# Kernel optimization log

Measured on AMD Instinct MI355X. Metric: run time of the kernel, lower is better.

Reference implementation:

```python
import jax, jax.numpy as jnp
import numpy as np

N_AGENTS = 10000
N_TARGETS = 10000
N_EDGES = 320000
IN_CH = 8
DS = 32          # n_channels // 2 per GAT preprocessor
NCH = 64         # n_channels
C = 128          # 2 * n_channels hidden width
OUT = 2
N_TAPS = 3
N_LAYERS = 2
RADIUS = 2.0
K_NBR = 10       # max_num_neighbors in radius_graph
BIG = 1e9


def radius_nbrs(qpos, kpos, radius, k, exclude_self):
    """For each query point, indices of <=k nearest key points within radius."""
    d2 = jnp.sum((qpos[:, None, :] - kpos[None, :, :]) ** 2, axis=-1)  # [Nq, Nk]
    if exclude_self:
        n = qpos.shape[0]
        d2 = d2.at[jnp.arange(n), jnp.arange(n)].set(BIG)
    d2 = jnp.where(d2 <= radius * radius, d2, BIG)
    negv, idx = jax.lax.top_k(-d2, k)   # nearest-k (deterministic stand-in for PyG's first-k)
    valid = negv > -BIG * 0.5           # [Nq, k] True where a real in-radius neighbor
    return idx, valid


def gatv2(src_feats, dst_feats, idx, valid, Wl, Wr, att, b):
    """Single-head GATv2Conv over a fixed-K neighbor list (idx indexes src_feats)."""
    xl = src_feats @ Wl                      # [Ns, H] messages
    xr = dst_feats @ Wr                      # [Nd, H]
    g = jax.nn.leaky_relu(xl[idx] + xr[:, None, :], 0.2)   # [Nd, K, H]
    s = jnp.einsum('nkh,h->nk', g, att)
    s = jnp.where(valid, s, -BIG)
    s = s - jnp.max(s, axis=1, keepdims=True)
    p = jnp.exp(s) * valid                   # masked exp; isolated nodes -> all-zero
    alpha = p / (jnp.sum(p, axis=1, keepdims=True) + 1e-16)
    return jnp.einsum('nk,nkh->nh', alpha, xl[idx]) + b


def graph_filter(x, src, dst, W, b, n):
    """Polynomial graph filter: y = sum_k S^k x W_k + b, S = unweighted adjacency."""
    y = x @ W[0]
    h = x
    for k in range(1, W.shape[0]):
        h = jax.ops.segment_sum(h[src], dst, num_segments=n)  # one shift tap
        y = y + h @ W[k]
    return y + b


def setup_inputs() -> dict:
    key = jax.random.key(0)
    ks = jax.random.split(key, 16)
    f32 = jnp.float32
    return {
        'own_obs': jax.random.normal(ks[0], (N_AGENTS, IN_CH), dtype=f32),
        'agent_positions': jax.random.uniform(ks[1], (N_AGENTS, 2), dtype=f32) * 100.0,
        'target_positions': jax.random.uniform(ks[2], (N_TARGETS, 2), dtype=f32) * 100.0,
        'W_self': jax.random.normal(ks[3], (IN_CH, NCH), dtype=f32) * 0.1,
        'b_self': jnp.zeros((NCH,), f32),
        'ag_Wl': jax.random.normal(ks[4], (2, DS), dtype=f32) * 0.1,
        'ag_Wr': jax.random.normal(ks[5], (2, DS), dtype=f32) * 0.1,
        'ag_att': jax.random.normal(ks[6], (DS,), dtype=f32) * 0.1,
        'ag_b': jnp.zeros((DS,), f32),
        'tg_Wl': jax.random.normal(ks[7], (2, DS), dtype=f32) * 0.1,
        'tg_Wr': jax.random.normal(ks[8], (2, DS), dtype=f32) * 0.1,
        'tg_att': jax.random.normal(ks[9], (DS,), dtype=f32) * 0.1,
        'tg_b': jnp.zeros((DS,), f32),
        'gf_W': jax.random.normal(ks[10], (N_LAYERS, N_TAPS + 1, C, C), dtype=f32) * (1.0 / np.sqrt(C)),
        'gf_b': jnp.zeros((N_LAYERS, C), f32),
        'bn_gamma': jnp.ones((N_LAYERS, C), f32),
        'bn_beta': jnp.zeros((N_LAYERS, C), f32),
        'W_read': jax.random.normal(ks[11], (C, OUT), dtype=f32) * 0.1,
        'b_read': jnp.zeros((OUT,), f32),
        'edge_index': jax.random.randint(ks[12], (2, N_EDGES), 0, N_AGENTS, dtype=jnp.int32),
    }


def reference(own_obs, agent_positions, target_positions, W_self, b_self,
              ag_Wl, ag_Wr, ag_att, ag_b, tg_Wl, tg_Wr, tg_att, tg_b,
              gf_W, gf_b, bn_gamma, bn_beta, W_read, b_read, edge_index):
    n = agent_positions.shape[0]
    # dynamic radius graphs (agent-agent; target->agent)
    a_idx, a_valid = radius_nbrs(agent_positions, agent_positions, RADIUS, K_NBR, True)
    t_idx, t_valid = radius_nbrs(agent_positions, target_positions, RADIUS, K_NBR, False)

    s = own_obs @ W_self + b_self                                            # self MLP (1 layer)
    a = gatv2(agent_positions, agent_positions, a_idx, a_valid, ag_Wl, ag_Wr, ag_att, ag_b)
    t = gatv2(target_positions, agent_positions, t_idx, t_valid, tg_Wl, tg_Wr, tg_att, tg_b)
    x = jnp.concatenate([s, a, t], axis=1)                                   # [N, 128]

    src, dst = edge_index[0], edge_index[1]
    for l in range(N_LAYERS):
        h = graph_filter(x, src, dst, gf_W[l], gf_b[l], n)
        mu = jnp.mean(h, axis=0)
        var = jnp.var(h, axis=0)
        h = (h - mu) / jnp.sqrt(var + 1e-5) * bn_gamma[l] + bn_beta[l]       # BatchNorm
        x = x + jax.nn.leaky_relu(h, 0.01)                                   # residual block
    return x @ W_read + b_read
```

## Files before the change

### kernel.cpp

```cpp
#include <hip/hip_runtime.h>

typedef unsigned long long u64;
typedef unsigned int u32;
typedef unsigned short ushort_t;

#define NA 10000
#define NE 320000
#define KN 10
#define GRID 50
#define NCELL (GRID * GRID)

typedef __attribute__((ext_vector_type(8))) short short8v;
typedef __attribute__((ext_vector_type(4))) float f32x4;

__device__ __forceinline__ u32 f2bf(float f) {
  union { float f; u32 u; } v; v.f = f;
  return (v.u + 0x7fffu + ((v.u >> 16) & 1u)) >> 16;
}
__device__ __forceinline__ float bf2f(u32 b) {
  union { u32 u; float f; } v; v.u = b << 16;
  return v.f;
}

__device__ __forceinline__ void insert10(u64* top, u64 key) {
#pragma unroll
  for (int t = 9; t > 0; --t) {
    u64 prev = top[t - 1];
    u64 cur = top[t];
    top[t] = (key < prev) ? prev : ((key < cur) ? key : cur);
  }
  top[0] = (key < top[0]) ? key : top[0];
}

__device__ __forceinline__ int cell_of(float2 p) {
  int cx = (int)(p.x * 0.5f);
  int cy = (int)(p.y * 0.5f);
  cx = min(max(cx, 0), GRID - 1);
  cy = min(max(cy, 0), GRID - 1);
  return cy * GRID + cx;
}

__global__ __launch_bounds__(256) void k_hist_self(const int* __restrict__ edst,
                                                   const float2* __restrict__ apos,
                                                   const float2* __restrict__ tpos,
                                                   int* __restrict__ deg, int* __restrict__ chist,
                                                   const float* __restrict__ own_obs,
                                                   const float* __restrict__ W_self, const float* __restrict__ b_self,
                                                   float* __restrict__ x,
                                                   const float* __restrict__ gfW,
                                                   ushort_t* __restrict__ Wh, ushort_t* __restrict__ Wlo) {
  __shared__ float sW[512], sb[64];
  int t = threadIdx.x;
  for (int i = t; i < 512; i += 256) sW[i] = W_self[i];
  if (t < 64) sb[t] = b_self[t];
  __syncthreads();
  int i = blockIdx.x * 256 + t;
  if (i < NE) {
    atomicAdd(&deg[edst[i]], 1);
  } else if (i < NE + 2 * NA) {
    int ii = i - NE;
    int graph = (ii >= NA) ? 1 : 0;
    int idx = ii - graph * NA;
    float2 p = graph ? tpos[idx] : apos[idx];
    atomicAdd(&chist[graph * NCELL + cell_of(p)], 1);
  } else if (i < NE + 2 * NA + 8 * NA) {
    int gid = i - NE - 2 * NA;
    int q = gid >> 3;
    int c8 = (gid & 7) * 8;
    const float4* op = (const float4*)(own_obs + (size_t)q * 8);
    float4 o0 = op[0], o1 = op[1];
    float obs[8] = {o0.x, o0.y, o0.z, o0.w, o1.x, o1.y, o1.z, o1.w};
    float out[8];
#pragma unroll
    for (int jj = 0; jj < 8; ++jj) {
      int c = c8 + jj;
      float s = sb[c];
#pragma unroll
      for (int k = 0; k < 8; ++k) s += obs[k] * sW[k * 64 + c];
      out[jj] = s;
    }
    float* xrow = x + (size_t)q * 128 + c8;
    *(float4*)(xrow) = make_float4(out[0], out[1], out[2], out[3]);
    *(float4*)(xrow + 4) = make_float4(out[4], out[5], out[6], out[7]);
  } else if (i < NE + 2 * NA + 8 * NA + 131072) {
    int w = i - NE - 2 * NA - 8 * NA;
    int l = w >> 16;
    int rem = w & 65535;
    int tt = rem >> 14;
    int k = (rem >> 7) & 127;
    int n = rem & 127;
    float v = gfW[(size_t)w];
    int kt = k >> 5;
    int hi = (k >> 3) & 3;
    int j = k & 7;
    int ct = n >> 4;
    int lane = hi * 16 + (n & 15);
    size_t dst = (((((size_t)(l * 4 + tt) * 4 + kt) * 8 + ct) * 64 + lane) * 8 + j);
    u32 h = f2bf(v);
    float r = v - bf2f(h);
    Wh[dst] = (ushort_t)h;
    Wlo[dst] = (ushort_t)f2bf(r);
  }
}

__global__ __launch_bounds__(1024) void k_scan_all(const int* __restrict__ deg, int* __restrict__ rp,
                                                   const int* __restrict__ chist, int* __restrict__ crp) {
  __shared__ int part[1024];
  int t = threadIdx.x;
  const int* in;
  int* out;
  int per, tot;
  if (blockIdx.x == 0) { in = deg; out = rp; per = 10; tot = NA; }
  else { in = chist; out = crp; per = 5; tot = 2 * NCELL; }
  int beg = min(t * per, tot), end = min(beg + per, tot);
  int s = 0;
  for (int i = beg; i < end; ++i) s += in[i];
  part[t] = s;
  __syncthreads();
  for (int o = 1; o < 1024; o <<= 1) {
    int v = part[t];
    int u = (t >= o) ? part[t - o] : 0;
    __syncthreads();
    part[t] = v + u;
    __syncthreads();
  }
  int base = (t > 0) ? part[t - 1] : 0;
  for (int i = beg; i < end; ++i) { out[i] = base; base += in[i]; }
  if (t == 1023) out[tot] = part[1023];
}

__global__ __launch_bounds__(256) void k_scatter_all(const int* __restrict__ esrc, const int* __restrict__ edst,
                                                     const int* __restrict__ rp, int* __restrict__ cur,
                                                     int* __restrict__ col,
                                                     const float2* __restrict__ apos, const float2* __restrict__ tpos,
                                                     const int* __restrict__ crp, int* __restrict__ ccur,
                                                     float2* __restrict__ ps, int* __restrict__ pid) {
  int i = blockIdx.x * 256 + threadIdx.x;
  if (i < NE) {
    int d = edst[i];
    int p = atomicAdd(&cur[d], 1);
    col[rp[d] + p] = esrc[i];
  } else if (i < NE + 2 * NA) {
    int ii = i - NE;
    int graph = (ii >= NA) ? 1 : 0;
    int idx = ii - graph * NA;
    float2 p = graph ? tpos[idx] : apos[idx];
    int gc = graph * NCELL + cell_of(p);
    int o = crp[gc] + atomicAdd(&ccur[gc], 1);
    ps[o] = p;
    pid[o] = idx;
  }
}

__global__ __launch_bounds__(256) void k_nbr_gat(const float2* __restrict__ apos, const float2* __restrict__ tpos,
                                                 const int* __restrict__ crp,
                                                 const float2* __restrict__ ps, const int* __restrict__ pid,
                                                 const float* __restrict__ agWl, const float* __restrict__ agWr,
                                                 const float* __restrict__ agatt, const float* __restrict__ agb,
                                                 const float* __restrict__ tgWl, const float* __restrict__ tgWr,
                                                 const float* __restrict__ tgatt, const float* __restrict__ tgb,
                                                 float* __restrict__ x) {
  __shared__ float sWl[2][64], sWr[2][64], satt[2][32], sbb[2][32];
  int t = threadIdx.x;
  if (t < 64) { sWl[0][t] = agWl[t]; sWr[0][t] = agWr[t]; sWl[1][t] = tgWl[t]; sWr[1][t] = tgWr[t]; }
  else if (t < 96) {
    int u = t - 64;
    satt[0][u] = agatt[u]; sbb[0][u] = agb[u]; satt[1][u] = tgatt[u]; sbb[1][u] = tgb[u];
  }
  __syncthreads();
  int tid = blockIdx.x * 256 + t;
  if (tid >= 2 * NA) return;
  int graph = (tid >= NA) ? 1 : 0;
  int q = tid - graph * NA;
  float2 qp = apos[q];
  int cx = min(max((int)(qp.x * 0.5f), 0), GRID - 1);
  int cy = min(max((int)(qp.y * 0.5f), 0), GRID - 1);

  u64 top[10];
#pragma unroll
  for (int k = 0; k < 10; ++k) top[k] = ~0ull;

  int x0 = max(cx - 1, 0), x1 = min(cx + 1, GRID - 1);
  int y0 = max(cy - 1, 0), y1 = min(cy + 1, GRID - 1);
  for (int yy = y0; yy <= y1; ++yy) {
    int cb = graph * NCELL + yy * GRID + x0;
    int ce = graph * NCELL + yy * GRID + x1;
    int b = crp[cb], e = crp[ce + 1];
    for (int j = b; j < e; ++j) {
      float2 kp = ps[j];
      float dx = qp.x - kp.x;
      float dy = qp.y - kp.y;
      float d2 = __fadd_rn(__fmul_rn(dx, dx), __fmul_rn(dy, dy));
      int g = pid[j];
      if (d2 <= 4.0f && !(graph == 0 && g == q)) {
        u64 key = ((u64)__float_as_uint(d2) << 32) | (u32)g;
        if (key < top[9]) insert10(top, key);
      }
    }
  }
  int cnt = 0;
#pragma unroll
  for (int k = 0; k < 10; ++k) cnt += (top[k] != ~0ull) ? 1 : 0;
  int idx[10];
#pragma unroll
  for (int k = 0; k < 10; ++k) idx[k] = (k < cnt) ? (int)(u32)(top[k] & 0xffffffffu) : 0;

  const float2* srcpos = graph ? tpos : apos;
  const float* wl = sWl[graph];
  const float* wr = sWr[graph];
  const float* at = satt[graph];
  const float* bb = sbb[graph];
  float xr[32];
#pragma unroll
  for (int c = 0; c < 32; ++c) xr[c] = qp.x * wr[c] + qp.y * wr[32 + c];
  float pv[10];
  float m = -1e30f;
#pragma unroll
  for (int k = 0; k < 10; ++k) {
    float2 p = srcpos[idx[k]];
    float s = 0.f;
#pragma unroll
    for (int c = 0; c < 32; ++c) {
      float xl = p.x * wl[c] + p.y * wl[32 + c];
      float g = xl + xr[c];
      g = (g >= 0.f) ? g : 0.2f * g;
      s += at[c] * g;
    }
    pv[k] = s;
    m = (k < cnt) ? fmaxf(m, s) : m;
  }
  float sum = 0.f;
#pragma unroll
  for (int k = 0; k < 10; ++k) {
    float e = (k < cnt) ? expf(pv[k] - m) : 0.f;
    pv[k] = e;
    sum += e;
  }
  float inv = 1.f / (sum + 1e-16f);
  float out[32];
#pragma unroll
  for (int c = 0; c < 32; ++c) out[c] = bb[c];
#pragma unroll
  for (int k = 0; k < 10; ++k) {
    float a = pv[k] * inv;
    float2 p = srcpos[idx[k]];
#pragma unroll
    for (int c = 0; c < 32; ++c) {
      float xl = p.x * wl[c] + p.y * wl[32 + c];
      out[c] += a * xl;
    }
  }
  float* xrow = x + (size_t)q * 128 + (graph ? 96 : 64);
#pragma unroll
  for (int c4 = 0; c4 < 8; ++c4)
    *(float4*)(xrow + c4 * 4) = make_float4(out[c4 * 4], out[c4 * 4 + 1], out[c4 * 4 + 2], out[c4 * 4 + 3]);
}

__global__ __launch_bounds__(256) void k_shift4(const float* __restrict__ xin, float* __restrict__ xout,
                                                const int* __restrict__ rp, const int* __restrict__ col) {
  int bid = blockIdx.x;
  int half = (bid & 7) >> 2;
  int slot = (bid >> 3) * 4 + (bid & 3);
  if (slot >= 1250) return;
  int hw = threadIdx.x >> 5;
  int li = threadIdx.x & 31;
  int row = slot * 8 + hw;
  int beg = rp[row], end = rp[row + 1];
  const float2* x2 = (const float2*)xin;
  int base = half * 32 + li;
  float2 acc = {0.f, 0.f};
  int j = beg;
  for (; j + 3 < end; j += 4) {
    int s0 = col[j], s1 = col[j + 1], s2 = col[j + 2], s3 = col[j + 3];
    float2 v0 = x2[(size_t)s0 * 64 + base];
    float2 v1 = x2[(size_t)s1 * 64 + base];
    float2 v2 = x2[(size_t)s2 * 64 + base];
    float2 v3 = x2[(size_t)s3 * 64 + base];
    acc.x += v0.x; acc.y += v0.y;
    acc.x += v1.x; acc.y += v1.y;
    acc.x += v2.x; acc.y += v2.y;
    acc.x += v3.x; acc.y += v3.y;
  }
  for (; j < end; ++j) {
    float2 v = x2[(size_t)col[j] * 64 + base];
    acc.x += v.x; acc.y += v.y;
  }
  ((float2*)xout)[(size_t)row * 64 + base] = acc;
}

__global__ __launch_bounds__(256) void k_gemm_mfma3(const float* __restrict__ a0, const float* __restrict__ a1,
                                                    const float* __restrict__ a2, const float* __restrict__ a3,
                                                    const ushort_t* __restrict__ Wh, const ushort_t* __restrict__ Wlo,
                                                    const float* __restrict__ b, float* __restrict__ y,
                                                    double* __restrict__ parts) {
  const int lane = threadIdx.x & 63;
  const int wave = threadIdx.x >> 6;
  const int ct0 = wave * 2;
  const int row = lane & 15;
  const int hi = lane >> 4;
  const int rb = blockIdx.x * 16;

  f32x4 acc[2];
#pragma unroll
  for (int c = 0; c < 2; ++c) {
    float bv = b[(ct0 + c) * 16 + row];
    acc[c][0] = bv; acc[c][1] = bv; acc[c][2] = bv; acc[c][3] = bv;
  }

  const float* aps[4] = {a0, a1, a2, a3};
#pragma unroll
  for (int t = 0; t < 4; ++t) {
    const float* at = aps[t];
#pragma unroll
    for (int kt = 0; kt < 4; ++kt) {
      const float* ap = at + (size_t)(rb + row) * 128 + kt * 32 + hi * 8;
      float4 fa = *(const float4*)(ap);
      float4 fb = *(const float4*)(ap + 4);
      float av[8] = {fa.x, fa.y, fa.z, fa.w, fb.x, fb.y, fb.z, fb.w};
      short8v ah, al;
#pragma unroll
      for (int j = 0; j < 8; ++j) {
        u32 h = f2bf(av[j]);
        float r = av[j] - bf2f(h);
        ah[j] = (short)h;
        al[j] = (short)f2bf(r);
      }
#pragma unroll
      for (int c = 0; c < 2; ++c) {
        size_t widx = ((((size_t)t * 4 + kt) * 8 + (ct0 + c)) * 64 + lane) * 8;
        short8v bh = *(const short8v*)(Wh + widx);
        short8v bl = *(const short8v*)(Wlo + widx);
        acc[c] = __builtin_amdgcn_mfma_f32_16x16x32_bf16(ah, bh, acc[c], 0, 0, 0);
        acc[c] = __builtin_amdgcn_mfma_f32_16x16x32_bf16(al, bh, acc[c], 0, 0, 0);
        acc[c] = __builtin_amdgcn_mfma_f32_16x16x32_bf16(ah, bl, acc[c], 0, 0, 0);
      }
    }
  }

#pragma unroll
  for (int c = 0; c < 2; ++c) {
#pragma unroll
    for (int r = 0; r < 4; ++r) {
      int grow = rb + hi * 4 + r;
      y[(size_t)grow * 128 + (ct0 + c) * 16 + row] = acc[c][r];
    }
  }

#pragma unroll
  for (int c = 0; c < 2; ++c) {
    double s = 0.0, ss = 0.0;
#pragma unroll
    for (int r = 0; r < 4; ++r) {
      double v = (double)acc[c][r];
      s += v;
      ss += v * v;
    }
    s += __shfl_xor(s, 16);
    ss += __shfl_xor(ss, 16);
    s += __shfl_xor(s, 32);
    ss += __shfl_xor(ss, 32);
    if (hi == 0) {
      int ch = (ct0 + c) * 16 + row;
      parts[(size_t)ch * 625 + blockIdx.x] = s;
      parts[(size_t)(128 + ch) * 625 + blockIdx.x] = ss;
    }
  }
}

__global__ __launch_bounds__(256) void k_bnfin(const double* __restrict__ parts,
                                               const float* __restrict__ gamma, const float* __restrict__ beta,
                                               float* __restrict__ AB) {
  __shared__ double s0[256], s1[256];
  int ch = blockIdx.x;
  int t = threadIdx.x;
  const double* ps = parts + (size_t)ch * 625;
  const double* pq = parts + (size_t)(128 + ch) * 625;
  double a = 0.0, b = 0.0;
  for (int i = t; i < 625; i += 256) { a += ps[i]; b += pq[i]; }
  s0[t] = a;
  s1[t] = b;
  __syncthreads();
  for (int o = 128; o > 0; o >>= 1) {
    if (t < o) { s0[t] += s0[t + o]; s1[t] += s1[t + o]; }
    __syncthreads();
  }
  if (t == 0) {
    double mu = s0[0] / (double)NA;
    double var = s1[0] / (double)NA - mu * mu;
    double rs = 1.0 / sqrt(var + 1e-5);
    AB[ch] = (float)rs * gamma[ch];
    AB[128 + ch] = beta[ch] - (float)(mu * rs) * gamma[ch];
  }
}

__global__ __launch_bounds__(256) void k_bnapply(const float* __restrict__ y, const float* __restrict__ AB,
                                                 const float* __restrict__ Wread, const float* __restrict__ bread,
                                                 float* __restrict__ x, float* __restrict__ out, int doread) {
  __shared__ float sAB[256], sWr[256];
  int t = threadIdx.x;
  sAB[t] = AB[t];
  sWr[t] = Wread[t];
  __syncthreads();
  const int n4 = NA * 32;
  for (int i = blockIdx.x * 256 + t; i < n4; i += gridDim.x * 256) {
    float4 yv = ((const float4*)y)[i];
    int c = (i & 31) * 4;
    float v0 = yv.x * sAB[c + 0] + sAB[128 + c + 0];
    float v1 = yv.y * sAB[c + 1] + sAB[128 + c + 1];
    float v2 = yv.z * sAB[c + 2] + sAB[128 + c + 2];
    float v3 = yv.w * sAB[c + 3] + sAB[128 + c + 3];
    v0 = (v0 >= 0.f) ? v0 : 0.01f * v0;
    v1 = (v1 >= 0.f) ? v1 : 0.01f * v1;
    v2 = (v2 >= 0.f) ? v2 : 0.01f * v2;
    v3 = (v3 >= 0.f) ? v3 : 0.01f * v3;
    float4 xv = ((float4*)x)[i];
    xv.x += v0; xv.y += v1; xv.z += v2; xv.w += v3;
    ((float4*)x)[i] = xv;
    if (doread) {
      float a0 = xv.x * sWr[(c + 0) * 2] + xv.y * sWr[(c + 1) * 2] + xv.z * sWr[(c + 2) * 2] + xv.w * sWr[(c + 3) * 2];
      float a1 = xv.x * sWr[(c + 0) * 2 + 1] + xv.y * sWr[(c + 1) * 2 + 1] + xv.z * sWr[(c + 2) * 2 + 1] + xv.w * sWr[(c + 3) * 2 + 1];
#pragma unroll
      for (int o = 1; o < 32; o <<= 1) {
        a0 += __shfl_xor(a0, o);
        a1 += __shfl_xor(a1, o);
      }
      if ((i & 31) == 0) {
        int row = i >> 5;
        out[row * 2 + 0] = a0 + bread[0];
        out[row * 2 + 1] = a1 + bread[1];
      }
    }
  }
}

extern "C" void kernel_launch(void* const* d_in, const int* in_sizes, int n_in,
                              void* d_out, int out_size, void* d_ws, size_t ws_size,
                              hipStream_t stream) {
  (void)in_sizes; (void)n_in; (void)out_size; (void)ws_size;
  const float* own_obs = (const float*)d_in[0];
  const float2* apos = (const float2*)d_in[1];
  const float2* tpos = (const float2*)d_in[2];
  const float* W_self = (const float*)d_in[3];
  const float* b_self = (const float*)d_in[4];
  const float* agWl = (const float*)d_in[5];
  const float* agWr = (const float*)d_in[6];
  const float* agatt = (const float*)d_in[7];
  const float* agb = (const float*)d_in[8];
  const float* tgWl = (const float*)d_in[9];
  const float* tgWr = (const float*)d_in[10];
  const float* tgatt = (const float*)d_in[11];
  const float* tgb = (const float*)d_in[12];
  const float* gfW = (const float*)d_in[13];
  const float* gfb = (const float*)d_in[14];
  const float* bng = (const float*)d_in[15];
  const float* bnb = (const float*)d_in[16];
  const float* Wread = (const float*)d_in[17];
  const float* bread = (const float*)d_in[18];
  const int* ei = (const int*)d_in[19];
  const int* esrc = ei;
  const int* edst = ei + NE;

  char* w = (char*)d_ws;
  size_t off = 0;
  auto take = [&](size_t bytes) -> void* {
    void* p = w + off;
    off += (bytes + 255) & ~(size_t)255;
    return p;
  };
  float* x = (float*)take((size_t)NA * 128 * 4);
  float* y = (float*)take((size_t)NA * 128 * 4);
  float* sh1 = (float*)take((size_t)NA * 128 * 4);
  float* sh2 = (float*)take((size_t)NA * 128 * 4);
  float* sh3 = (float*)take((size_t)NA * 128 * 4);
  ushort_t* Wh = (ushort_t*)take((size_t)131072 * 2);
  ushort_t* Wlo = (ushort_t*)take((size_t)131072 * 2);
  double* parts = (double*)take((size_t)256 * 625 * 8);
  float* AB = (float*)take(256 * 4);
  int* deg = (int*)take((size_t)NA * 4);
  int* cur = (int*)take((size_t)NA * 4);
  int* chist = (int*)take((size_t)2 * NCELL * 4);
  int* ccur = (int*)take((size_t)2 * NCELL * 4);
  int* rp = (int*)take((size_t)(NA + 1) * 4);
  int* col = (int*)take((size_t)NE * 4);
  int* crp = (int*)take((size_t)(2 * NCELL + 1) * 4);
  float2* ps = (float2*)take((size_t)2 * NA * 8);
  int* pid = (int*)take((size_t)2 * NA * 4);

  hipMemsetAsync(deg, 0, (size_t)((char*)(ccur + 2 * NCELL) - (char*)deg), stream);
  k_hist_self<<<(NE + 2 * NA + 8 * NA + 131072 + 255) / 256, 256, 0, stream>>>(
      edst, apos, tpos, deg, chist, own_obs, W_self, b_self, x, gfW, Wh, Wlo);
  k_scan_all<<<2, 1024, 0, stream>>>(deg, rp, chist, crp);
  k_scatter_all<<<(NE + 2 * NA + 255) / 256, 256, 0, stream>>>(esrc, edst, rp, cur, col,
                                                               apos, tpos, crp, ccur, ps, pid);
  k_nbr_gat<<<(2 * NA + 255) / 256, 256, 0, stream>>>(apos, tpos, crp, ps, pid,
                                                      agWl, agWr, agatt, agb, tgWl, tgWr, tgatt, tgb, x);

  for (int l = 0; l < 2; ++l) {
    const ushort_t* Whl = Wh + (size_t)l * 65536;
    const ushort_t* Wll = Wlo + (size_t)l * 65536;
    const float* bl = gfb + (size_t)l * 128;
    const float* gl = bng + (size_t)l * 128;
    const float* bb = bnb + (size_t)l * 128;
    k_shift4<<<2504, 256, 0, stream>>>(x, sh1, rp, col);
    k_shift4<<<2504, 256, 0, stream>>>(sh1, sh2, rp, col);
    k_shift4<<<2504, 256, 0, stream>>>(sh2, sh3, rp, col);
    k_gemm_mfma3<<<NA / 16, 256, 0, stream>>>(x, sh1, sh2, sh3, Whl, Wll, bl, y, parts);
    k_bnfin<<<128, 256, 0, stream>>>(parts, gl, bb, AB);
    k_bnapply<<<256, 256, 0, stream>>>(y, AB, Wread, bread, x, (float*)d_out, l == 1 ? 1 : 0);
  }
}
```

Before: 280.5 us.

## Widen shift gather to float4 per lane and process two row tiles per GEMM block

The sparse shift kernel now gathers 16-byte float4 chunks per lane, with 16 lanes covering half a row and four rows per wave, instead of float2 with 32 lanes per row. It also uses a 2-way unroll and a nontemporal store. The MFMA GEMM now computes 32 rows per block (two 16-row tiles), so each bf16 hi/lo weight fragment load is reused across two tiles. The partial-stat buffer shrinks to 313 blocks. This cuts weight reloads and instruction count per gathered byte, at the cost of more registers and fewer blocks for the GEMM.

```diff
diff --git a/kernel.cpp b/kernel.cpp
--- a/kernel.cpp
+++ b/kernel.cpp
@@ -9,6 +9,7 @@
 #define KN 10
 #define GRID 50
 #define NCELL (GRID * GRID)
+#define GB 313
 
 typedef __attribute__((ext_vector_type(8))) short short8v;
 typedef __attribute__((ext_vector_type(4))) float f32x4;
@@ -256,36 +257,31 @@
     *(float4*)(xrow + c4 * 4) = make_float4(out[c4 * 4], out[c4 * 4 + 1], out[c4 * 4 + 2], out[c4 * 4 + 3]);
 }
 
-__global__ __launch_bounds__(256) void k_shift4(const float* __restrict__ xin, float* __restrict__ xout,
+__global__ __launch_bounds__(256) void k_shift3(const float* __restrict__ xin, float* __restrict__ xout,
                                                 const int* __restrict__ rp, const int* __restrict__ col) {
   int bid = blockIdx.x;
   int half = (bid & 7) >> 2;
   int slot = (bid >> 3) * 4 + (bid & 3);
-  if (slot >= 1250) return;
-  int hw = threadIdx.x >> 5;
-  int li = threadIdx.x & 31;
-  int row = slot * 8 + hw;
+  if (slot >= 625) return;
+  int wid = threadIdx.x >> 6;
+  int lane = threadIdx.x & 63;
+  int q = lane >> 4;
+  int li = lane & 15;
+  int row = slot * 16 + wid * 4 + q;
   int beg = rp[row], end = rp[row + 1];
-  const float2* x2 = (const float2*)xin;
-  int base = half * 32 + li;
-  float2 acc = {0.f, 0.f};
+  const f32x4* x4 = (const f32x4*)xin;
+  int base = half * 16 + li;
+  f32x4 acc = {0.f, 0.f, 0.f, 0.f};
   int j = beg;
-  for (; j + 3 < end; j += 4) {
-    int s0 = col[j], s1 = col[j + 1], s2 = col[j + 2], s3 = col[j + 3];
-    float2 v0 = x2[(size_t)s0 * 64 + base];
-    float2 v1 = x2[(size_t)s1 * 64 + base];
-    float2 v2 = x2[(size_t)s2 * 64 + base];
-    float2 v3 = x2[(size_t)s3 * 64 + base];
-    acc.x += v0.x; acc.y += v0.y;
-    acc.x += v1.x; acc.y += v1.y;
-    acc.x += v2.x; acc.y += v2.y;
-    acc.x += v3.x; acc.y += v3.y;
-  }
-  for (; j < end; ++j) {
-    float2 v = x2[(size_t)col[j] * 64 + base];
-    acc.x += v.x; acc.y += v.y;
-  }
-  ((float2*)xout)[(size_t)row * 64 + base] = acc;
+  for (; j + 1 < end; j += 2) {
+    int s0 = col[j], s1 = col[j + 1];
+    f32x4 v0 = x4[(size_t)s0 * 32 + base];
+    f32x4 v1 = x4[(size_t)s1 * 32 + base];
+    acc += v0;
+    acc += v1;
+  }
+  if (j < end) acc += x4[(size_t)col[j] * 32 + base];
+  __builtin_nontemporal_store(acc, &((f32x4*)xout)[(size_t)row * 32 + base]);
 }
 
 __global__ __launch_bounds__(256) void k_gemm_mfma3(const float* __restrict__ a0, const float* __restrict__ a1,
@@ -298,13 +294,15 @@
   const int ct0 = wave * 2;
   const int row = lane & 15;
   const int hi = lane >> 4;
-  const int rb = blockIdx.x * 16;
-
-  f32x4 acc[2];
+  const int rb = blockIdx.x * 32;
+  const bool rt1ok = (rb + 16) < NA;
+
+  f32x4 acc[2][2];
 #pragma unroll
   for (int c = 0; c < 2; ++c) {
     float bv = b[(ct0 + c) * 16 + row];
-    acc[c][0] = bv; acc[c][1] = bv; acc[c][2] = bv; acc[c][3] = bv;
+    acc[0][c][0] = bv; acc[0][c][1] = bv; acc[0][c][2] = bv; acc[0][c][3] = bv;
+    acc[1][c][0] = bv; acc[1][c][1] = bv; acc[1][c][2] = bv; acc[1][c][3] = bv;
   }
 
   const float* aps[4] = {a0, a1, a2, a3};
@@ -313,36 +311,61 @@
     const float* at = aps[t];
 #pragma unroll
     for (int kt = 0; kt < 4; ++kt) {
-      const float* ap = at + (size_t)(rb + row) * 128 + kt * 32 + hi * 8;
-      float4 fa = *(const float4*)(ap);
-      float4 fb = *(const float4*)(ap + 4);
-      float av[8] = {fa.x, fa.y, fa.z, fa.w, fb.x, fb.y, fb.z, fb.w};
-      short8v ah, al;
-#pragma unroll
-      for (int j = 0; j < 8; ++j) {
-        u32 h = f2bf(av[j]);
-        float r = av[j] - bf2f(h);
-        ah[j] = (short)h;
-        al[j] = (short)f2bf(r);
+      short8v ah0, al0, ah1, al1;
+      {
+        const float* ap = at + (size_t)(rb + row) * 128 + kt * 32 + hi * 8;
+        float4 fa = *(const float4*)(ap);
+        float4 fb = *(const float4*)(ap + 4);
+        float av[8] = {fa.x, fa.y, fa.z, fa.w, fb.x, fb.y, fb.z, fb.w};
+#pragma unroll
+        for (int j = 0; j < 8; ++j) {
+          u32 h = f2bf(av[j]);
+          float r = av[j] - bf2f(h);
+          ah0[j] = (short)h;
+          al0[j] = (short)f2bf(r);
+        }
+      }
+      if (rt1ok) {
+        const float* ap = at + (size_t)(rb + 16 + row) * 128 + kt * 32 + hi * 8;
+        float4 fa = *(const float4*)(ap);
+        float4 fb = *(const float4*)(ap + 4);
+        float av[8] = {fa.x, fa.y, fa.z, fa.w, fb.x, fb.y, fb.z, fb.w};
+#pragma unroll
+        for (int j = 0; j < 8; ++j) {
+          u32 h = f2bf(av[j]);
+          float r = av[j] - bf2f(h);
+          ah1[j] = (short)h;
+          al1[j] = (short)f2bf(r);
+        }
+      } else {
+#pragma unroll
+        for (int j = 0; j < 8; ++j) { ah1[j] = 0; al1[j] = 0; }
       }
 #pragma unroll
       for (int c = 0; c < 2; ++c) {
         size_t widx = ((((size_t)t * 4 + kt) * 8 + (ct0 + c)) * 64 + lane) * 8;
         short8v bh = *(const short8v*)(Wh + widx);
         short8v bl = *(const short8v*)(Wlo + widx);
-        acc[c] = __builtin_amdgcn_mfma_f32_16x16x32_bf16(ah, bh, acc[c], 0, 0, 0);
-        acc[c] = __builtin_amdgcn_mfma_f32_16x16x32_bf16(al, bh, acc[c], 0, 0, 0);
-        acc[c] = __builtin_amdgcn_mfma_f32_16x16x32_bf16(ah, bl, acc[c], 0, 0, 0);
-      }
-    }
-  }
-
-#pragma unroll
-  for (int c = 0; c < 2; ++c) {
-#pragma unroll
-    for (int r = 0; r < 4; ++r) {
-      int grow = rb + hi * 4 + r;
-      y[(size_t)grow * 128 + (ct0 + c) * 16 + row] = acc[c][r];
+        acc[0][c] = __builtin_amdgcn_mfma_f32_16x16x32_bf16(ah0, bh, acc[0][c], 0, 0, 0);
+        acc[0][c] = __builtin_amdgcn_mfma_f32_16x16x32_bf16(al0, bh, acc[0][c], 0, 0, 0);
+        acc[0][c] = __builtin_amdgcn_mfma_f32_16x16x32_bf16(ah0, bl, acc[0][c], 0, 0, 0);
+        acc[1][c] = __builtin_amdgcn_mfma_f32_16x16x32_bf16(ah1, bh, acc[1][c], 0, 0, 0);
+        acc[1][c] = __builtin_amdgcn_mfma_f32_16x16x32_bf16(al1, bh, acc[1][c], 0, 0, 0);
+        acc[1][c] = __builtin_amdgcn_mfma_f32_16x16x32_bf16(ah1, bl, acc[1][c], 0, 0, 0);
+      }
+    }
+  }
+
+#pragma unroll
+  for (int rt = 0; rt < 2; ++rt) {
+    if (rt == 1 && !rt1ok) break;
+#pragma unroll
+    for (int c = 0; c < 2; ++c) {
+#pragma unroll
+      for (int r = 0; r < 4; ++r) {
+        int grow = rb + rt * 16 + hi * 4 + r;
+        y[(size_t)grow * 128 + (ct0 + c) * 16 + row] = acc[rt][c][r];
+      }
     }
   }
 
@@ -351,9 +374,17 @@
     double s = 0.0, ss = 0.0;
 #pragma unroll
     for (int r = 0; r < 4; ++r) {
-      double v = (double)acc[c][r];
+      double v = (double)acc[0][c][r];
       s += v;
       ss += v * v;
+    }
+    if (rt1ok) {
+#pragma unroll
+      for (int r = 0; r < 4; ++r) {
+        double v = (double)acc[1][c][r];
+        s += v;
+        ss += v * v;
+      }
     }
     s += __shfl_xor(s, 16);
     ss += __shfl_xor(ss, 16);
@@ -361,8 +392,8 @@
     ss += __shfl_xor(ss, 32);
     if (hi == 0) {
       int ch = (ct0 + c) * 16 + row;
-      parts[(size_t)ch * 625 + blockIdx.x] = s;
-      parts[(size_t)(128 + ch) * 625 + blockIdx.x] = ss;
+      parts[(size_t)ch * GB + blockIdx.x] = s;
+      parts[(size_t)(128 + ch) * GB + blockIdx.x] = ss;
     }
   }
 }
@@ -373,10 +404,10 @@
   __shared__ double s0[256], s1[256];
   int ch = blockIdx.x;
   int t = threadIdx.x;
-  const double* ps = parts + (size_t)ch * 625;
-  const double* pq = parts + (size_t)(128 + ch) * 625;
+  const double* ps = parts + (size_t)ch * GB;
+  const double* pq = parts + (size_t)(128 + ch) * GB;
   double a = 0.0, b = 0.0;
-  for (int i = t; i < 625; i += 256) { a += ps[i]; b += pq[i]; }
+  for (int i = t; i < GB; i += 256) { a += ps[i]; b += pq[i]; }
   s0[t] = a;
   s1[t] = b;
   __syncthreads();
@@ -474,7 +505,7 @@
   float* sh3 = (float*)take((size_t)NA * 128 * 4);
   ushort_t* Wh = (ushort_t*)take((size_t)131072 * 2);
   ushort_t* Wlo = (ushort_t*)take((size_t)131072 * 2);
-  double* parts = (double*)take((size_t)256 * 625 * 8);
+  double* parts = (double*)take((size_t)256 * GB * 8);
   float* AB = (float*)take(256 * 4);
   int* deg = (int*)take((size_t)NA * 4);
   int* cur = (int*)take((size_t)NA * 4);
@@ -501,10 +532,10 @@
     const float* bl = gfb + (size_t)l * 128;
     const float* gl = bng + (size_t)l * 128;
     const float* bb = bnb + (size_t)l * 128;
-    k_shift4<<<2504, 256, 0, stream>>>(x, sh1, rp, col);
-    k_shift4<<<2504, 256, 0, stream>>>(sh1, sh2, rp, col);
-    k_shift4<<<2504, 256, 0, stream>>>(sh2, sh3, rp, col);
-    k_gemm_mfma3<<<NA / 16, 256, 0, stream>>>(x, sh1, sh2, sh3, Whl, Wll, bl, y, parts);
+    k_shift3<<<1256, 256, 0, stream>>>(x, sh1, rp, col);
+    k_shift3<<<1256, 256, 0, stream>>>(sh1, sh2, rp, col);
+    k_shift3<<<1256, 256, 0, stream>>>(sh2, sh3, rp, col);
+    k_gemm_mfma3<<<GB, 256, 0, stream>>>(x, sh1, sh2, sh3, Whl, Wll, bl, y, parts);
     k_bnfin<<<128, 256, 0, stream>>>(parts, gl, bb, AB);
     k_bnapply<<<256, 256, 0, stream>>>(y, AB, Wread, bread, x, (float*)d_out, l == 1 ? 1 : 0);
   }
```

After: 259.6 us. -7.5%, faster.

## Fuse three shift taps into one cooperative kernel with grid syncs and float4 gathers

Applied to the files above, without the earlier changes.

Replaces the three separate shift-tap launches per layer with a single cooperative kernel that runs all three taps, separated by grid-wide syncs. The gather is widened from float2 to float4 per lane, with 16 lanes per row, and outputs are written with nontemporal stores. The aim is to remove two kernel launches and their gaps per layer and to issue fewer, wider memory requests. In exchange it depends on all 1256 blocks being co-resident, adds grid-sync cost, and unrolls the inner loop less deeply.

```diff
diff --git a/kernel.cpp b/kernel.cpp
--- a/kernel.cpp
+++ b/kernel.cpp
@@ -1,4 +1,7 @@
 #include <hip/hip_runtime.h>
+#include <hip/hip_cooperative_groups.h>
+
+namespace cg = cooperative_groups;
 
 typedef unsigned long long u64;
 typedef unsigned int u32;
@@ -9,6 +12,7 @@
 #define KN 10
 #define GRID 50
 #define NCELL (GRID * GRID)
+#define GB 625
 
 typedef __attribute__((ext_vector_type(8))) short short8v;
 typedef __attribute__((ext_vector_type(4))) float f32x4;
@@ -256,36 +260,42 @@
     *(float4*)(xrow + c4 * 4) = make_float4(out[c4 * 4], out[c4 * 4 + 1], out[c4 * 4 + 2], out[c4 * 4 + 3]);
 }
 
-__global__ __launch_bounds__(256) void k_shift4(const float* __restrict__ xin, float* __restrict__ xout,
-                                                const int* __restrict__ rp, const int* __restrict__ col) {
+__device__ __forceinline__ void shift_body(const float* __restrict__ xin, float* __restrict__ xout,
+                                           const int* __restrict__ rp, const int* __restrict__ col) {
   int bid = blockIdx.x;
   int half = (bid & 7) >> 2;
   int slot = (bid >> 3) * 4 + (bid & 3);
-  if (slot >= 1250) return;
-  int hw = threadIdx.x >> 5;
-  int li = threadIdx.x & 31;
-  int row = slot * 8 + hw;
+  if (slot >= 625) return;
+  int wid = threadIdx.x >> 6;
+  int lane = threadIdx.x & 63;
+  int q = lane >> 4;
+  int li = lane & 15;
+  int row = slot * 16 + wid * 4 + q;
   int beg = rp[row], end = rp[row + 1];
-  const float2* x2 = (const float2*)xin;
-  int base = half * 32 + li;
-  float2 acc = {0.f, 0.f};
+  const f32x4* x4 = (const f32x4*)xin;
+  int base = half * 16 + li;
+  f32x4 acc = {0.f, 0.f, 0.f, 0.f};
   int j = beg;
-  for (; j + 3 < end; j += 4) {
-    int s0 = col[j], s1 = col[j + 1], s2 = col[j + 2], s3 = col[j + 3];
-    float2 v0 = x2[(size_t)s0 * 64 + base];
-    float2 v1 = x2[(size_t)s1 * 64 + base];
-    float2 v2 = x2[(size_t)s2 * 64 + base];
-    float2 v3 = x2[(size_t)s3 * 64 + base];
-    acc.x += v0.x; acc.y += v0.y;
-    acc.x += v1.x; acc.y += v1.y;
-    acc.x += v2.x; acc.y += v2.y;
-    acc.x += v3.x; acc.y += v3.y;
-  }
-  for (; j < end; ++j) {
-    float2 v = x2[(size_t)col[j] * 64 + base];
-    acc.x += v.x; acc.y += v.y;
-  }
-  ((float2*)xout)[(size_t)row * 64 + base] = acc;
+  for (; j + 1 < end; j += 2) {
+    int s0 = col[j], s1 = col[j + 1];
+    f32x4 v0 = x4[(size_t)s0 * 32 + base];
+    f32x4 v1 = x4[(size_t)s1 * 32 + base];
+    acc += v0;
+    acc += v1;
+  }
+  if (j < end) acc += x4[(size_t)col[j] * 32 + base];
+  __builtin_nontemporal_store(acc, &((f32x4*)xout)[(size_t)row * 32 + base]);
+}
+
+__global__ __launch_bounds__(256) void k_shift_coop(const float* __restrict__ x, float* __restrict__ sh1,
+                                                    float* __restrict__ sh2, float* __restrict__ sh3,
+                                                    const int* __restrict__ rp, const int* __restrict__ col) {
+  cg::grid_group g = cg::this_grid();
+  shift_body(x, sh1, rp, col);
+  g.sync();
+  shift_body(sh1, sh2, rp, col);
+  g.sync();
+  shift_body(sh2, sh3, rp, col);
 }
 
 __global__ __launch_bounds__(256) void k_gemm_mfma3(const float* __restrict__ a0, const float* __restrict__ a1,
@@ -361,8 +371,8 @@
     ss += __shfl_xor(ss, 32);
     if (hi == 0) {
       int ch = (ct0 + c) * 16 + row;
-      parts[(size_t)ch * 625 + blockIdx.x] = s;
-      parts[(size_t)(128 + ch) * 625 + blockIdx.x] = ss;
+      parts[(size_t)ch * GB + blockIdx.x] = s;
+      parts[(size_t)(128 + ch) * GB + blockIdx.x] = ss;
     }
   }
 }
@@ -373,10 +383,10 @@
   __shared__ double s0[256], s1[256];
   int ch = blockIdx.x;
   int t = threadIdx.x;
-  const double* ps = parts + (size_t)ch * 625;
-  const double* pq = parts + (size_t)(128 + ch) * 625;
+  const double* ps = parts + (size_t)ch * GB;
+  const double* pq = parts + (size_t)(128 + ch) * GB;
   double a = 0.0, b = 0.0;
-  for (int i = t; i < 625; i += 256) { a += ps[i]; b += pq[i]; }
+  for (int i = t; i < GB; i += 256) { a += ps[i]; b += pq[i]; }
   s0[t] = a;
   s1[t] = b;
   __syncthreads();
@@ -474,7 +484,7 @@
   float* sh3 = (float*)take((size_t)NA * 128 * 4);
   ushort_t* Wh = (ushort_t*)take((size_t)131072 * 2);
   ushort_t* Wlo = (ushort_t*)take((size_t)131072 * 2);
-  double* parts = (double*)take((size_t)256 * 625 * 8);
+  double* parts = (double*)take((size_t)256 * GB * 8);
   float* AB = (float*)take(256 * 4);
   int* deg = (int*)take((size_t)NA * 4);
   int* cur = (int*)take((size_t)NA * 4);
@@ -501,10 +511,11 @@
     const float* bl = gfb + (size_t)l * 128;
     const float* gl = bng + (size_t)l * 128;
     const float* bb = bnb + (size_t)l * 128;
-    k_shift4<<<2504, 256, 0, stream>>>(x, sh1, rp, col);
-    k_shift4<<<2504, 256, 0, stream>>>(sh1, sh2, rp, col);
-    k_shift4<<<2504, 256, 0, stream>>>(sh2, sh3, rp, col);
-    k_gemm_mfma3<<<NA / 16, 256, 0, stream>>>(x, sh1, sh2, sh3, Whl, Wll, bl, y, parts);
+    {
+      void* args[] = {(void*)&x, (void*)&sh1, (void*)&sh2, (void*)&sh3, (void*)&rp, (void*)&col};
+      hipLaunchCooperativeKernel((const void*)k_shift_coop, dim3(1256), dim3(256), args, 0, stream);
+    }
+    k_gemm_mfma3<<<GB, 256, 0, stream>>>(x, sh1, sh2, sh3, Whl, Wll, bl, y, parts);
     k_bnfin<<<128, 256, 0, stream>>>(parts, gl, bb, AB);
     k_bnapply<<<256, 256, 0, stream>>>(y, AB, Wread, bread, x, (float*)d_out, l == 1 ? 1 : 0);
   }
```

Result: slower. 844.3 us (+201.0%).
